# Kernel optimization log

Hardware: AMD Instinct MI355X
Metric: run time of the kernel (lower is better)

Reference implementation:

```python
import jax, jax.numpy as jnp
import numpy as np


def setup_inputs() -> dict:
    key = jax.random.key(0)
    k1, k2 = jax.random.split(key)
    n, c, H, W = 8, 16, 512, 512
    pred = jax.random.normal(k1, (n, c, H, W), dtype=jnp.float32)
    target = jax.random.randint(k2, (n, H, W), 0, c, dtype=jnp.int64)
    weights = jnp.ones((n, 1, H, W), dtype=jnp.float32)  # ignored by the module
    return {"pred": pred, "target": target, "weights": weights}


def reference(pred, target, weights):
    # pred: [n,c,H,W] logits; target: [n,H,W] int class ids; weights arg is ignored
    n, c, H, W = pred.shape
    # Global (whole-batch) per-class pixel counts -> inverse-frequency weights.
    counts = jnp.zeros((c,), dtype=pred.dtype).at[target.reshape(-1)].add(1.0)
    w_class = jnp.where(counts > 0, 1.0 / (counts * c), 0.0)  # [c]
    w = w_class[target]  # [n,H,W] per-pixel weight (constant w.r.t. pred)
    # log-softmax gathered at target class per pixel
    logp = jax.nn.log_softmax(pred, axis=1)  # [n,c,H,W]
    lp_t = jnp.take_along_axis(logp, target[:, None, :, :], axis=1)[:, 0]  # [n,H,W]
    num = (lp_t * w).reshape(n, -1).sum(axis=1)  # [n]
    den = w.reshape(n, -1).sum(axis=1)           # [n]
    return -(num / den).mean()
```

## Files before the change

### kernel.cpp

```cpp
#include <hip/hip_runtime.h>
#include <stdint.h>

#define NIMG 8
#define NCLS 16
#define HW   262144
#define PXB  512
#define NBLK 4096

__device__ __forceinline__ void g2lds16(const float* g, float* l) {
    __builtin_amdgcn_global_load_lds(
        (const __attribute__((address_space(1))) unsigned int*)g,
        (__attribute__((address_space(3))) unsigned int*)l,
        16, 0, 0);
}

__global__ __launch_bounds__(256) void dwce_main(const float* __restrict__ pred,
                                                 const int* __restrict__ tgt,
                                                 float* __restrict__ partials) {
    __shared__ float tile[NCLS * PXB];
    __shared__ float s_bin[32];
    const int tid = threadIdx.x;

    const int b = blockIdx.x;
    const long long px0 = (long long)b * PXB;
    const int n_img = (int)(px0 >> 18);
    const int hw0   = (int)(px0 & (HW - 1));
    const float* base = pred + (size_t)n_img * NCLS * HW + hw0;

    const int w    = tid >> 6;
    const int lane = tid & 63;
    const int loff = lane * 4;

#pragma unroll
    for (int j = 0; j < 4; ++j) {
        const int c = w * 4 + j;
        const float* gc = base + (size_t)c * HW;
        float* lc = &tile[c * PXB];
        g2lds16(gc + loff,       lc + loff);
        g2lds16(gc + 256 + loff, lc + 256 + loff);
    }

    if (tid < 32) s_bin[tid] = 0.0f;
    const int2 t2 = *(const int2*)(tgt + px0 + tid * 2);

    __syncthreads();

    const int p = tid * 2;

    float2 m  = make_float2(-3.0e38f, -3.0e38f);
    float2 xt = make_float2(0.f, 0.f);
#pragma unroll
    for (int c = 0; c < NCLS; ++c) {
        const float2 v = *(const float2*)&tile[c * PXB + p];
        m.x = fmaxf(m.x, v.x);
        m.y = fmaxf(m.y, v.y);
        if (t2.x == c) xt.x = v.x;
        if (t2.y == c) xt.y = v.y;
    }

    float2 s = make_float2(0.f, 0.f);
#pragma unroll
    for (int c = 0; c < NCLS; ++c) {
        const float2 v = *(const float2*)&tile[c * PXB + p];
        s.x += __expf(v.x - m.x);
        s.y += __expf(v.y - m.y);
    }

    const float lp0 = xt.x - (m.x + __logf(s.x));
    const float lp1 = xt.y - (m.y + __logf(s.y));

    atomicAdd(&s_bin[t2.x], lp0);
    atomicAdd(&s_bin[t2.y], lp1);
    atomicAdd(&s_bin[16 + t2.x], 1.0f);
    atomicAdd(&s_bin[16 + t2.y], 1.0f);

    __syncthreads();
    if (tid < 32)
        partials[(size_t)tid * NBLK + b] = s_bin[tid];
}

__global__ __launch_bounds__(256) void dwce_final(const float* __restrict__ ws,
                                                  float* __restrict__ out) {
    __shared__ float tot[32][NIMG];
    __shared__ float wcl[NCLS];
    __shared__ float ratio[NIMG];
    const int tid = threadIdx.x;
    const int c = tid >> 3;
    const int n = tid & 7;

    const float4* p = (const float4*)(ws + (size_t)c * NBLK + n * 512);
    float4 a = make_float4(0.f, 0.f, 0.f, 0.f);
#pragma unroll 8
    for (int k = 0; k < 128; ++k) {
        float4 q = p[k];
        a.x += q.x; a.y += q.y; a.z += q.z; a.w += q.w;
    }
    tot[c][n] = (a.x + a.y) + (a.z + a.w);
    __syncthreads();

    if (tid < NCLS) {
        float g = 0.f;
#pragma unroll
        for (int i = 0; i < NIMG; ++i) g += tot[NCLS + tid][i];
        wcl[tid] = (g > 0.f) ? 1.0f / (g * (float)NCLS) : 0.0f;
    }
    __syncthreads();
    if (tid < NIMG) {
        float num = 0.f, den = 0.f;
#pragma unroll
        for (int c2 = 0; c2 < NCLS; ++c2) {
            num += tot[c2][tid] * wcl[c2];
            den += tot[NCLS + c2][tid] * wcl[c2];
        }
        ratio[tid] = num / den;
    }
    __syncthreads();
    if (tid == 0) {
        float r = 0.f;
#pragma unroll
        for (int i = 0; i < NIMG; ++i) r += ratio[i];
        out[0] = -r * (1.0f / (float)NIMG);
    }
}

extern "C" void kernel_launch(void* const* d_in, const int* in_sizes, int n_in,
                              void* d_out, int out_size, void* d_ws, size_t ws_size,
                              hipStream_t stream) {
    const float* pred = (const float*)d_in[0];
    const int*   tgt  = (const int*)d_in[1];
    float* out = (float*)d_out;
    float* ws  = (float*)d_ws;

    dwce_main<<<NBLK, 256, 0, stream>>>(pred, tgt, ws);
    dwce_final<<<1, 256, 0, stream>>>(ws, out);
}
```

Before: 215.2 us.

## Halve block pixel tile, one pixel per thread, drop max-subtraction in softmax

Measured after the change: 228.5 us. 6.2% more time.

```diff
diff --git a/kernel.cpp b/kernel.cpp
--- a/kernel.cpp
+++ b/kernel.cpp
@@ -1,11 +1,10 @@
 #include <hip/hip_runtime.h>
-#include <stdint.h>
 
 #define NIMG 8
 #define NCLS 16
 #define HW   262144
-#define PXB  512
-#define NBLK 4096
+#define PXB  256
+#define NBLK 8192
 
 __device__ __forceinline__ void g2lds16(const float* g, float* l) {
     __builtin_amdgcn_global_load_lds(
@@ -14,9 +13,9 @@
         16, 0, 0);
 }
 
-__global__ __launch_bounds__(256) void dwce_main(const float* __restrict__ pred,
-                                                 const int* __restrict__ tgt,
-                                                 float* __restrict__ partials) {
+__global__ __launch_bounds__(256, 8) void dwce_main(const float* __restrict__ pred,
+                                                    const int* __restrict__ tgt,
+                                                    float* __restrict__ partials) {
     __shared__ float tile[NCLS * PXB];
     __shared__ float s_bin[32];
     const int tid = threadIdx.x;
@@ -34,45 +33,26 @@
 #pragma unroll
     for (int j = 0; j < 4; ++j) {
         const int c = w * 4 + j;
-        const float* gc = base + (size_t)c * HW;
-        float* lc = &tile[c * PXB];
-        g2lds16(gc + loff,       lc + loff);
-        g2lds16(gc + 256 + loff, lc + 256 + loff);
+        g2lds16(base + (size_t)c * HW + loff, &tile[c * PXB] + loff);
     }
 
     if (tid < 32) s_bin[tid] = 0.0f;
-    const int2 t2 = *(const int2*)(tgt + px0 + tid * 2);
+    const int t = tgt[px0 + tid];
 
     __syncthreads();
 
-    const int p = tid * 2;
-
-    float2 m  = make_float2(-3.0e38f, -3.0e38f);
-    float2 xt = make_float2(0.f, 0.f);
+    float s  = 0.0f;
+    float xt = 0.0f;
 #pragma unroll
     for (int c = 0; c < NCLS; ++c) {
-        const float2 v = *(const float2*)&tile[c * PXB + p];
-        m.x = fmaxf(m.x, v.x);
-        m.y = fmaxf(m.y, v.y);
-        if (t2.x == c) xt.x = v.x;
-        if (t2.y == c) xt.y = v.y;
+        const float v = tile[c * PXB + tid];
+        s += __expf(v);
+        if (t == c) xt = v;
     }
+    const float lp = xt - __logf(s);
 
-    float2 s = make_float2(0.f, 0.f);
-#pragma unroll
-    for (int c = 0; c < NCLS; ++c) {
-        const float2 v = *(const float2*)&tile[c * PXB + p];
-        s.x += __expf(v.x - m.x);
-        s.y += __expf(v.y - m.y);
-    }
-
-    const float lp0 = xt.x - (m.x + __logf(s.x));
-    const float lp1 = xt.y - (m.y + __logf(s.y));
-
-    atomicAdd(&s_bin[t2.x], lp0);
-    atomicAdd(&s_bin[t2.y], lp1);
-    atomicAdd(&s_bin[16 + t2.x], 1.0f);
-    atomicAdd(&s_bin[16 + t2.y], 1.0f);
+    atomicAdd(&s_bin[t], lp);
+    atomicAdd(&s_bin[16 + t], 1.0f);
 
     __syncthreads();
     if (tid < 32)
@@ -88,10 +68,10 @@
     const int c = tid >> 3;
     const int n = tid & 7;
 
-    const float4* p = (const float4*)(ws + (size_t)c * NBLK + n * 512);
+    const float4* p = (const float4*)(ws + (size_t)c * NBLK + n * 1024);
     float4 a = make_float4(0.f, 0.f, 0.f, 0.f);
 #pragma unroll 8
-    for (int k = 0; k < 128; ++k) {
+    for (int k = 0; k < 256; ++k) {
         float4 q = p[k];
         a.x += q.x; a.y += q.y; a.z += q.z; a.w += q.w;
     }
```
